# Kernel optimization log

Measured on AMD Instinct MI355X. Metric: run time of the kernel, lower is better.

The kernel has to match this reference:

```python
import jax, jax.numpy as jnp
import numpy as np

B, S1, S2, DV = 64, 1024, 1024, 256

def setup_inputs() -> dict:
    key0 = jax.random.key(0)
    k1, k2, k3, k4, k5 = jax.random.split(key0, 5)
    return {
        "x": jax.random.normal(k1, (B, S1, 3), dtype=jnp.float32),
        "key": jax.random.normal(k2, (B, S2, 3), dtype=jnp.float32),
        "value": jax.random.normal(k3, (B, S2, DV), dtype=jnp.float32),
        "W": jax.random.normal(k4, (1, 6), dtype=jnp.float32) * (1.0 / np.sqrt(6.0)),
        "b": jax.random.normal(k5, (1,), dtype=jnp.float32) * 0.1,
    }

def reference(x, key, value, W, b):
    # Original: cat([x_rep, key_rep], -1) @ W^T + b == x @ W[:, :3]^T + key @ W[:, 3:]^T + b.
    # This avoids materializing the (B, S1, S2, 6) expanded tensor while computing identical math.
    w_x = W[0, :3]                      # (3,)
    w_k = W[0, 3:]                      # (3,)
    sx = jnp.einsum('bif,f->bi', x, w_x)      # (B, S1)
    sk = jnp.einsum('bjf,f->bj', key, w_k)    # (B, S2)
    scores = sx[:, :, None] + sk[:, None, :] + b[0]   # (B, S1, S2)
    attn = jax.nn.softmax(scores, axis=-1)            # softmax over S2
    return jnp.einsum('bij,bjd->bid', attn, value)    # (B, S1, DV)
```

## Files before the change

### kernel.cpp

```cpp
#include <hip/hip_runtime.h>


#define NB 64
#define S1V 1024
#define S2V 1024
#define DVV 256
#define NCHUNK 16
#define JPC (S2V / NCHUNK)

typedef float nf4 __attribute__((ext_vector_type(4)));


__global__ __launch_bounds__(256) void k_pv(const float* __restrict__ key,
                                            const float* __restrict__ value,
                                            const float* __restrict__ W,
                                            float* __restrict__ partial) {
    const int b     = blockIdx.x >> 4;
    const int chunk = blockIdx.x & (NCHUNK - 1);
    const int t     = threadIdx.x;
    const int wave  = t >> 6, lane = t & 63;

    const float wk0 = W[3], wk1 = W[4], wk2 = W[5];

    const float4* k4 = (const float4*)(key + (size_t)b * S2V * 3);
    float4 a = k4[3 * t + 0];
    float4 c = k4[3 * t + 1];
    float4 d = k4[3 * t + 2];
    float sk0 = fmaf(a.x, wk0, fmaf(a.y, wk1, a.z * wk2));
    float sk1 = fmaf(a.w, wk0, fmaf(c.x, wk1, c.y * wk2));
    float sk2 = fmaf(c.z, wk0, fmaf(c.w, wk1, d.x * wk2));
    float sk3 = fmaf(d.y, wk0, fmaf(d.z, wk1, d.w * wk2));

    __shared__ float redm[4], reds[4];

    float m = fmaxf(fmaxf(sk0, sk1), fmaxf(sk2, sk3));
    #pragma unroll
    for (int off = 32; off; off >>= 1) m = fmaxf(m, __shfl_xor(m, off));
    if (lane == 0) redm[wave] = m;
    __syncthreads();
    m = fmaxf(fmaxf(redm[0], redm[1]), fmaxf(redm[2], redm[3]));

    float e0 = __expf(sk0 - m), e1 = __expf(sk1 - m);
    float e2 = __expf(sk2 - m), e3 = __expf(sk3 - m);
    float s = e0 + e1 + e2 + e3;
    #pragma unroll
    for (int off = 32; off; off >>= 1) s += __shfl_xor(s, off);
    if (lane == 0) reds[wave] = s;
    __syncthreads();
    s = reds[0] + reds[1] + reds[2] + reds[3];
    const float inv = 1.0f / s;

    __shared__ float p_lds[JPC];
    const int tlo = chunk * (JPC / 4);
    if (t >= tlo && t < tlo + JPC / 4) {
        const int q = (t - tlo) * 4;
        p_lds[q + 0] = e0 * inv;
        p_lds[q + 1] = e1 * inv;
        p_lds[q + 2] = e2 * inv;
        p_lds[q + 3] = e3 * inv;
    }
    __syncthreads();

    const float4* v4 = (const float4*)(value + (size_t)b * S2V * DVV);
    const int jbase = chunk * JPC + wave * (JPC / 4);
    float4 acc = make_float4(0.f, 0.f, 0.f, 0.f);
    #pragma unroll
    for (int i = 0; i < JPC / 4; ++i) {
        const float pj = p_lds[wave * (JPC / 4) + i];
        float4 v = v4[(size_t)(jbase + i) * 64 + lane];
        acc.x = fmaf(pj, v.x, acc.x);
        acc.y = fmaf(pj, v.y, acc.y);
        acc.z = fmaf(pj, v.z, acc.z);
        acc.w = fmaf(pj, v.w, acc.w);
    }

    __shared__ float4 accl[256];
    accl[t] = acc;
    __syncthreads();
    if (wave == 0) {
        float4 r0 = accl[lane];
        float4 r1 = accl[64 + lane];
        float4 r2 = accl[128 + lane];
        float4 r3 = accl[192 + lane];
        r0.x += r1.x + r2.x + r3.x;
        r0.y += r1.y + r2.y + r3.y;
        r0.z += r1.z + r2.z + r3.z;
        r0.w += r1.w + r2.w + r3.w;
        ((float4*)(partial + ((size_t)b * NCHUNK + chunk) * DVV))[lane] = r0;
    }
}

__global__ __launch_bounds__(256) void k_out(const float* __restrict__ partial,
                                             float* __restrict__ out) {
    const int b    = blockIdx.x >> 7;
    const int rt   = blockIdx.x & 127;
    const int t    = threadIdx.x;
    const int d4   = t & 63;
    const int rsub = t >> 6;

    const float4* pp = (const float4*)(partial + (size_t)b * NCHUNK * DVV);
    float4 acc = make_float4(0.f, 0.f, 0.f, 0.f);
    #pragma unroll
    for (int c = rsub * 4; c < rsub * 4 + 4; ++c) {
        float4 v = pp[c * 64 + d4];
        acc.x += v.x; acc.y += v.y; acc.z += v.z; acc.w += v.w;
    }
    __shared__ float4 accl[256];
    accl[t] = acc;
    __syncthreads();
    float4 r = accl[d4];
    float4 r1 = accl[64 + d4];
    float4 r2 = accl[128 + d4];
    float4 r3 = accl[192 + d4];
    r.x += r1.x + r2.x + r3.x;
    r.y += r1.y + r2.y + r3.y;
    r.z += r1.z + r2.z + r3.z;
    r.w += r1.w + r2.w + r3.w;

    nf4 rv = { r.x, r.y, r.z, r.w };
    nf4* out4 = (nf4*)(out + ((size_t)b * S1V + (size_t)rt * 8) * DVV);
    __builtin_nontemporal_store(rv, &out4[(size_t)rsub * 64 + d4]);
    __builtin_nontemporal_store(rv, &out4[(size_t)(rsub + 4) * 64 + d4]);
}

extern "C" void kernel_launch(void* const* d_in, const int* in_sizes, int n_in,
                              void* d_out, int out_size, void* d_ws, size_t ws_size,
                              hipStream_t stream) {
    const float* key   = (const float*)d_in[1];
    const float* value = (const float*)d_in[2];
    const float* W     = (const float*)d_in[3];
    float* out = (float*)d_out;

    float* partial = (float*)d_ws;

    k_pv<<<NB * NCHUNK, 256, 0, stream>>>(key, value, W, partial);
    k_out<<<NB * 128, 256, 0, stream>>>(partial, out);
}
```

Measured before the change: 119.8 us.

## Fuse partial reduction and output broadcast into one kernel via inter-block flags

Merges the two launches into a single kernel. Each block publishes its per-chunk partial with a release-store flag, then spins until all 16 chunk flags of its batch are set, reduces the partials and writes 64 output rows. This removes the second launch and its dependency gap. In exchange it relies on every block of a batch being co-resident, and the flags are never reset between calls, so later calls may read partials before they are rewritten.

```diff
diff --git a/kernel.cpp b/kernel.cpp
--- a/kernel.cpp
+++ b/kernel.cpp
@@ -7,14 +7,17 @@
 #define DVV 256
 #define NCHUNK 16
 #define JPC (S2V / NCHUNK)
+#define FLAG_MAGIC 0x13579BDFu
 
 typedef float nf4 __attribute__((ext_vector_type(4)));
 
 
-__global__ __launch_bounds__(256) void k_pv(const float* __restrict__ key,
-                                            const float* __restrict__ value,
-                                            const float* __restrict__ W,
-                                            float* __restrict__ partial) {
+__global__ __launch_bounds__(256) void k_fused(const float* __restrict__ key,
+                                               const float* __restrict__ value,
+                                               const float* __restrict__ W,
+                                               float* __restrict__ partial,
+                                               unsigned int* __restrict__ flags,
+                                               float* __restrict__ out) {
     const int b     = blockIdx.x >> 4;
     const int chunk = blockIdx.x & (NCHUNK - 1);
     const int t     = threadIdx.x;
@@ -88,39 +91,39 @@
         r0.w += r1.w + r2.w + r3.w;
         ((float4*)(partial + ((size_t)b * NCHUNK + chunk) * DVV))[lane] = r0;
     }
-}
 
-__global__ __launch_bounds__(256) void k_out(const float* __restrict__ partial,
-                                             float* __restrict__ out) {
-    const int b    = blockIdx.x >> 7;
-    const int rt   = blockIdx.x & 127;
-    const int t    = threadIdx.x;
-    const int d4   = t & 63;
-    const int rsub = t >> 6;
+    __threadfence();
+    __syncthreads();
+    if (t == 0) {
+        __hip_atomic_store(&flags[b * NCHUNK + chunk], FLAG_MAGIC,
+                           __ATOMIC_RELEASE, __HIP_MEMORY_SCOPE_AGENT);
+    }
 
-    const float4* pp = (const float4*)(partial + (size_t)b * NCHUNK * DVV);
-    float4 acc = make_float4(0.f, 0.f, 0.f, 0.f);
+    {
+        const unsigned int* f = &flags[b * NCHUNK + (t & (NCHUNK - 1))];
+        while (__hip_atomic_load(f, __ATOMIC_ACQUIRE,
+                                 __HIP_MEMORY_SCOPE_AGENT) != FLAG_MAGIC) { }
+    }
+    __syncthreads();
+
+    float rsum = 0.f;
+    const float* pb = partial + (size_t)b * NCHUNK * DVV;
     #pragma unroll
-    for (int c = rsub * 4; c < rsub * 4 + 4; ++c) {
-        float4 v = pp[c * 64 + d4];
-        acc.x += v.x; acc.y += v.y; acc.z += v.z; acc.w += v.w;
+    for (int c2 = 0; c2 < NCHUNK; ++c2)
+        rsum += pb[c2 * DVV + t];
+
+    __shared__ float row_lds[DVV];
+    row_lds[t] = rsum;
+    __syncthreads();
+
+    nf4 rv = ((const nf4*)row_lds)[lane];
+
+    nf4* ob = (nf4*)(out + ((size_t)b * S1V + (size_t)chunk * JPC) * DVV);
+    #pragma unroll
+    for (int k = 0; k < 16; ++k) {
+        const int row = wave + k * 4;
+        __builtin_nontemporal_store(rv, &ob[(size_t)row * 64 + lane]);
     }
-    __shared__ float4 accl[256];
-    accl[t] = acc;
-    __syncthreads();
-    float4 r = accl[d4];
-    float4 r1 = accl[64 + d4];
-    float4 r2 = accl[128 + d4];
-    float4 r3 = accl[192 + d4];
-    r.x += r1.x + r2.x + r3.x;
-    r.y += r1.y + r2.y + r3.y;
-    r.z += r1.z + r2.z + r3.z;
-    r.w += r1.w + r2.w + r3.w;
-
-    nf4 rv = { r.x, r.y, r.z, r.w };
-    nf4* out4 = (nf4*)(out + ((size_t)b * S1V + (size_t)rt * 8) * DVV);
-    __builtin_nontemporal_store(rv, &out4[(size_t)rsub * 64 + d4]);
-    __builtin_nontemporal_store(rv, &out4[(size_t)(rsub + 4) * 64 + d4]);
 }
 
 extern "C" void kernel_launch(void* const* d_in, const int* in_sizes, int n_in,
@@ -131,8 +134,8 @@
     const float* W     = (const float*)d_in[3];
     float* out = (float*)d_out;
 
-    float* partial = (float*)d_ws;
+    float*        partial = (float*)d_ws;
+    unsigned int* flags   = (unsigned int*)((char*)d_ws + (1u << 20));
 
-    k_pv<<<NB * NCHUNK, 256, 0, stream>>>(key, value, W, partial);
-    k_out<<<NB * 128, 256, 0, stream>>>(partial, out);
+    k_fused<<<NB * NCHUNK, 256, 0, stream>>>(key, value, W, partial, flags, out);
 }
```

After: 338.3 us. 182% more time.
